# Optimization experiments

Hardware: AMD Instinct MI355X
Metric: run time of the kernel (lower is better)

Reference implementation:

```python
import jax, jax.numpy as jnp
import numpy as np

TEMP = 0.05
NUM_CLUSTERS = 8192  # labels.max()+1 in the original; fixed for jit-compat
EPS_SUM = 1e-6

def _l2norm(x):
    # F.normalize(x, dim=1): x / ||x||.clamp_min(1e-12)
    return x / jnp.maximum(jnp.linalg.norm(x, axis=1, keepdims=True), 1e-12)

def setup_inputs() -> dict:
    key = jax.random.key(0)
    k1, k2, k3, k4 = jax.random.split(key, 4)
    B, N, D = 1024, 131072, 256
    inputs = jax.random.normal(k1, (B, D), dtype=jnp.float32)
    features = jax.random.normal(k2, (N, D), dtype=jnp.float32)  # memory bank buffer
    indexes = jax.random.randint(k3, (B,), 0, N)
    labels = jax.random.randint(k4, (N,), 0, NUM_CLUSTERS)
    return {"inputs": inputs, "features": features, "indexes": indexes, "labels": labels}

def reference(inputs, features, indexes, labels):
    B = inputs.shape[0]
    inputs_norm = _l2norm(inputs)            # [B, D]
    features_norm = _l2norm(features)        # [N, D]
    # HM.forward: cosine similarity against the memory bank, then temperature
    logits = (inputs_norm @ features_norm.T) / TEMP          # [B, N]
    # label-grouped scatter-reduce: sim[c, b] = sum over samples s with label c of logits[b, s]
    sim = jax.ops.segment_sum(logits.T, labels, num_segments=NUM_CLUSTERS)  # [NC, B]
    nums = jax.ops.segment_sum(jnp.ones((labels.shape[0],), jnp.float32), labels,
                               num_segments=NUM_CLUSTERS)                   # [NC]
    mask = (nums > 0).astype(jnp.float32)                                   # [NC]
    denom = mask * nums + (1.0 - mask)
    sim = sim / denom[:, None]               # per-cluster mean similarity
    # masked softmax over clusters, per sample
    simT = sim.T                             # [B, NC]
    exps = jnp.exp(simT) * mask[None, :]
    p = exps / (jnp.sum(exps, axis=1, keepdims=True) + EPS_SUM)
    logp = jnp.log(p + 1e-6)                 # [B, NC]
    targets = labels[indexes]                # [B]
    loss = -jnp.mean(jnp.take_along_axis(logp, targets[:, None], axis=1))
    return loss
```

## Files before the change

kernel.cpp:

```cpp
#include <hip/hip_runtime.h>

#define BSZ   1024
#define NSZ   131072
#define DSZ   256
#define NC    8192
#define TEMPR 0.05f
#define CAP   64

typedef float f32x4_t __attribute__((ext_vector_type(4)));
typedef int   i32x4_t __attribute__((ext_vector_type(4)));

__device__ __forceinline__ unsigned short f2bf(float f) {
  unsigned u = __float_as_uint(f);
  u += 0x7fffu + ((u >> 16) & 1u);
  return (unsigned short)(u >> 16);
}

__device__ __forceinline__ void gload16(const unsigned short* g, unsigned short* l) {
  __builtin_amdgcn_global_load_lds(
      (const __attribute__((address_space(1))) unsigned int*)(g),
      (__attribute__((address_space(3))) unsigned int*)(l), 16, 0, 0);
}

#define ZERO_F4_COUNT 2308

__global__ __launch_bounds__(256) void k_norm(const float* __restrict__ in,
                                              unsigned short* __restrict__ anorm,
                                              float4* __restrict__ zero_region) {
  int gid  = blockIdx.x * 256 + threadIdx.x;
  if (gid < ZERO_F4_COUNT) zero_region[gid] = make_float4(0.f, 0.f, 0.f, 0.f);
  int wid  = gid >> 6;
  int lane = threadIdx.x & 63;
  float4 v = reinterpret_cast<const float4*>(in)[wid * 64 + lane];
  float ss = v.x * v.x + v.y * v.y + v.z * v.z + v.w * v.w;
#pragma unroll
  for (int off = 32; off; off >>= 1) ss += __shfl_xor(ss, off);
  float rn = 1.f / fmaxf(sqrtf(ss), 1e-12f);
  ushort4 ob = make_ushort4(f2bf(v.x * rn), f2bf(v.y * rn), f2bf(v.z * rn), f2bf(v.w * rn));
  reinterpret_cast<ushort4*>(anorm)[wid * 64 + lane] = ob;
}

__global__ __launch_bounds__(256) void k_fill(const int* __restrict__ labels,
                                              int* __restrict__ cnt,
                                              int* __restrict__ bucket) {
  int i = blockIdx.x * 256 + threadIdx.x;
  int lab = labels[i];
  int p = atomicAdd(&cnt[lab], 1);
  if (p < CAP) bucket[(lab << 6) + p] = i;
}

__global__ __launch_bounds__(256) void k_gather_sum(const float* __restrict__ feat,
                                                    const int* __restrict__ bucket,
                                                    const int* __restrict__ cnt,
                                                    unsigned short* __restrict__ cmean) {
  __shared__ float4 part[192];
  int c    = blockIdx.x;
  int lane = threadIdx.x & 63;
  int wv   = threadIdx.x >> 6;
  int n = cnt[c];
  n = n < CAP ? n : CAP;
  int j = wv + 4 * lane;
  int myidx = (j < n) ? bucket[(c << 6) + j] : 0;
  float4 acc = make_float4(0.f, 0.f, 0.f, 0.f);
  int iters = (n - wv + 3) >> 2;
  float4 v;
  if (iters > 0) {
    int s0 = __shfl(myidx, 0);
    v = reinterpret_cast<const float4*>(feat)[(size_t)s0 * 64 + lane];
  }
  for (int t = 0; t < iters; ++t) {
    float4 cur = v;
    if (t + 1 < iters) {
      int sn = __shfl(myidx, t + 1);
      v = reinterpret_cast<const float4*>(feat)[(size_t)sn * 64 + lane];
    }
    float ss = cur.x * cur.x + cur.y * cur.y + cur.z * cur.z + cur.w * cur.w;
#pragma unroll
    for (int off = 32; off; off >>= 1) ss += __shfl_xor(ss, off);
    float rn = 1.f / fmaxf(sqrtf(ss), 1e-12f);
    acc.x += cur.x * rn; acc.y += cur.y * rn; acc.z += cur.z * rn; acc.w += cur.w * rn;
  }
  if (wv > 0) part[(wv - 1) * 64 + lane] = acc;
  __syncthreads();
  if (wv == 0) {
    float4 p1 = part[lane], p2 = part[64 + lane], p3 = part[128 + lane];
    acc.x += p1.x + p2.x + p3.x;
    acc.y += p1.y + p2.y + p3.y;
    acc.z += p1.z + p2.z + p3.z;
    acc.w += p1.w + p2.w + p3.w;
    float den = n > 0 ? (float)n : 1.f;
    float sc = 1.f / (TEMPR * den);
    ushort4 ob = make_ushort4(f2bf(acc.x * sc), f2bf(acc.y * sc),
                              f2bf(acc.z * sc), f2bf(acc.w * sc));
    reinterpret_cast<ushort4*>(cmean)[c * 64 + lane] = ob;
  }
}

__global__ __launch_bounds__(256) void k_gemm(const unsigned short* __restrict__ A,
                                              const unsigned short* __restrict__ Bt,
                                              const int* __restrict__ cnt,
                                              const int* __restrict__ indexes,
                                              const int* __restrict__ labels,
                                              float* __restrict__ sumexp,
                                              float* __restrict__ tlogit,
                                              int* __restrict__ ticket,
                                              float* __restrict__ out) {
  __shared__ __align__(16) unsigned short a_lds[128 * 64];
  __shared__ __align__(16) unsigned short b_lds[128 * 64];
  __shared__ int t_lds[128];
  __shared__ float red[4];
  __shared__ int lastflag;

  const int tid  = threadIdx.x;
  const int bn0  = blockIdx.x * 128;
  const int bm0  = blockIdx.y * 128;
  const int lane = tid & 63;
  const int w    = tid >> 6;
  const int wr   = w >> 1, wc = w & 1;
  const int col16 = lane & 15, khalf = lane >> 4;

  if (tid < 128) t_lds[tid] = labels[indexes[bm0 + tid]];

  f32x4_t acc[4][4] = {};

#pragma unroll 1
  for (int kt = 0; kt < 4; ++kt) {
    const int k0 = kt * 64;
    __syncthreads();
#pragma unroll
    for (int j = 0; j < 4; ++j) {
      int c   = (j * 4 + w) * 64 + lane;
      int row = c >> 3;
      int lk  = (c & 7) ^ (row & 7);
      const unsigned short* gA = A  + (size_t)(bm0 + row) * DSZ + k0 + lk * 8;
      const unsigned short* gB = Bt + (size_t)(bn0 + row) * DSZ + k0 + lk * 8;
      gload16(gA, a_lds + (j * 4 + w) * 512);
      gload16(gB, b_lds + (j * 4 + w) * 512);
    }
    __syncthreads();

#pragma unroll
    for (int ks = 0; ks < 2; ++ks) {
      const int klocB = ks * 64 + khalf * 16;
      i32x4_t af[4], bf[4];
#pragma unroll
      for (int m = 0; m < 4; ++m) {
        int lr = wr * 64 + m * 16 + col16;
        int ab = (lr << 7) + (klocB ^ ((lr & 7) << 4));
        af[m] = *reinterpret_cast<const i32x4_t*>(reinterpret_cast<const char*>(a_lds) + ab);
      }
#pragma unroll
      for (int n = 0; n < 4; ++n) {
        int lc = wc * 64 + n * 16 + col16;
        int bb = (lc << 7) + (klocB ^ ((lc & 7) << 4));
        bf[n] = *reinterpret_cast<const i32x4_t*>(reinterpret_cast<const char*>(b_lds) + bb);
      }
#pragma unroll
      for (int m = 0; m < 4; ++m)
#pragma unroll
        for (int n = 0; n < 4; ++n)
          asm("v_mfma_f32_16x16x32_bf16 %0, %1, %2, %0" : "+v"(acc[m][n]) : "v"(af[m]), "v"(bf[n]));
    }
  }

#pragma unroll
  for (int m = 0; m < 4; ++m) {
    const int lr0 = wr * 64 + m * 16 + khalf * 4;
    float s0 = 0.f, s1 = 0.f, s2 = 0.f, s3 = 0.f;
#pragma unroll
    for (int n = 0; n < 4; ++n) {
      int gc = bn0 + wc * 64 + n * 16 + col16;
      float msk = cnt[gc] > 0 ? 1.f : 0.f;
      if (t_lds[lr0 + 0] == gc) tlogit[bm0 + lr0 + 0] = acc[m][n][0];
      if (t_lds[lr0 + 1] == gc) tlogit[bm0 + lr0 + 1] = acc[m][n][1];
      if (t_lds[lr0 + 2] == gc) tlogit[bm0 + lr0 + 2] = acc[m][n][2];
      if (t_lds[lr0 + 3] == gc) tlogit[bm0 + lr0 + 3] = acc[m][n][3];
      s0 += msk * __expf(acc[m][n][0]);
      s1 += msk * __expf(acc[m][n][1]);
      s2 += msk * __expf(acc[m][n][2]);
      s3 += msk * __expf(acc[m][n][3]);
    }
#pragma unroll
    for (int off = 1; off < 16; off <<= 1) {
      s0 += __shfl_xor(s0, off);
      s1 += __shfl_xor(s1, off);
      s2 += __shfl_xor(s2, off);
      s3 += __shfl_xor(s3, off);
    }
    if (col16 == 0) {
      atomicAdd(&sumexp[bm0 + lr0 + 0], s0);
      atomicAdd(&sumexp[bm0 + lr0 + 1], s1);
      atomicAdd(&sumexp[bm0 + lr0 + 2], s2);
      atomicAdd(&sumexp[bm0 + lr0 + 3], s3);
    }
  }

  __syncthreads();
  if (tid == 0) {
    int t = __hip_atomic_fetch_add(ticket, 1, __ATOMIC_ACQ_REL, __HIP_MEMORY_SCOPE_AGENT);
    lastflag = (t == 511);
  }
  __syncthreads();
  if (lastflag) {
    float lp = 0.f;
    for (int r = tid; r < BSZ; r += 256) {
      float tl = __uint_as_float(__hip_atomic_load((const unsigned*)&tlogit[r],
                                 __ATOMIC_RELAXED, __HIP_MEMORY_SCOPE_AGENT));
      float se = __uint_as_float(__hip_atomic_load((const unsigned*)&sumexp[r],
                                 __ATOMIC_RELAXED, __HIP_MEMORY_SCOPE_AGENT));
      float p = __expf(tl) / (se + 1e-6f);
      lp += logf(p + 1e-6f);
    }
#pragma unroll
    for (int off = 32; off; off >>= 1) lp += __shfl_xor(lp, off);
    if (lane == 0) red[w] = lp;
    __syncthreads();
    if (tid == 0) out[0] = -(red[0] + red[1] + red[2] + red[3]) * (1.0f / (float)BSZ);
  }
}

#define OFF_ANORM   0u
#define OFF_CMEAN   524288u
#define OFF_BUCKET  (OFF_CMEAN + 4194304u)
#define OFF_TLOGIT  (OFF_BUCKET + 2097152u)
#define OFF_CNT     (OFF_TLOGIT + 4096u)
#define OFF_SUMEXP  (OFF_CNT + 32768u)
#define OFF_TICKET  (OFF_SUMEXP + 4096u)

extern "C" void kernel_launch(void* const* d_in, const int* in_sizes, int n_in,
                              void* d_out, int out_size, void* d_ws, size_t ws_size,
                              hipStream_t stream) {
  const float* inputs   = (const float*)d_in[0];
  const float* features = (const float*)d_in[1];
  const int*   indexes  = (const int*)d_in[2];
  const int*   labels   = (const int*)d_in[3];
  float* out = (float*)d_out;

  char* ws = (char*)d_ws;
  unsigned short* anorm   = (unsigned short*)(ws + OFF_ANORM);
  unsigned short* cmean   = (unsigned short*)(ws + OFF_CMEAN);
  int*            bucket  = (int*)(ws + OFF_BUCKET);
  float*          tlogit  = (float*)(ws + OFF_TLOGIT);
  int*            cnt     = (int*)(ws + OFF_CNT);
  float*          sumexp  = (float*)(ws + OFF_SUMEXP);
  int*            ticket  = (int*)(ws + OFF_TICKET);

  k_norm<<<256, 256, 0, stream>>>(inputs, anorm, (float4*)(ws + OFF_CNT));
  k_fill<<<NSZ / 256, 256, 0, stream>>>(labels, cnt, bucket);
  k_gather_sum<<<NC, 256, 0, stream>>>(features, bucket, cnt, cmean);
  k_gemm<<<dim3(NC / 128, BSZ / 128), 256, 0, stream>>>(anorm, cmean, cnt, indexes,
                                                        labels, sumexp, tlogit,
                                                        ticket, out);
}
```

Baseline: 68.26 us.

## Double-buffer GEMM LDS tiles, vectorize label fill, two clusters per gather block

The GEMM kernel now double-buffers its A/B LDS tiles, issuing the global-to-LDS loads for the next K step before computing on the current one, so each iteration needs one barrier instead of two. k_fill loads labels as int4 and does four atomics per thread, launching a quarter of the blocks. k_gather_sum handles two clusters per block with interleaved loads to raise memory-level parallelism. The GEMM LDS footprint doubles, which may lower occupancy. Bucket insertion order changes, so the float summation order of the cluster means can differ.

```diff
diff --git a/kernel.cpp b/kernel.cpp
--- a/kernel.cpp
+++ b/kernel.cpp
@@ -43,56 +43,79 @@
 __global__ __launch_bounds__(256) void k_fill(const int* __restrict__ labels,
                                               int* __restrict__ cnt,
                                               int* __restrict__ bucket) {
-  int i = blockIdx.x * 256 + threadIdx.x;
-  int lab = labels[i];
-  int p = atomicAdd(&cnt[lab], 1);
-  if (p < CAP) bucket[(lab << 6) + p] = i;
+  int gid = blockIdx.x * 256 + threadIdx.x;
+  int4 l = reinterpret_cast<const int4*>(labels)[gid];
+  int base = gid * 4;
+  int p0 = atomicAdd(&cnt[l.x], 1);
+  int p1 = atomicAdd(&cnt[l.y], 1);
+  int p2 = atomicAdd(&cnt[l.z], 1);
+  int p3 = atomicAdd(&cnt[l.w], 1);
+  if (p0 < CAP) bucket[(l.x << 6) + p0] = base + 0;
+  if (p1 < CAP) bucket[(l.y << 6) + p1] = base + 1;
+  if (p2 < CAP) bucket[(l.z << 6) + p2] = base + 2;
+  if (p3 < CAP) bucket[(l.w << 6) + p3] = base + 3;
 }
 
 __global__ __launch_bounds__(256) void k_gather_sum(const float* __restrict__ feat,
                                                     const int* __restrict__ bucket,
                                                     const int* __restrict__ cnt,
                                                     unsigned short* __restrict__ cmean) {
-  __shared__ float4 part[192];
-  int c    = blockIdx.x;
-  int lane = threadIdx.x & 63;
-  int wv   = threadIdx.x >> 6;
-  int n = cnt[c];
-  n = n < CAP ? n : CAP;
+  __shared__ float4 part[2][192];
+  const int lane = threadIdx.x & 63;
+  const int wv   = threadIdx.x >> 6;
+  const int c0   = blockIdx.x * 2;
+  int n0 = cnt[c0];     n0 = n0 < CAP ? n0 : CAP;
+  int n1 = cnt[c0 + 1]; n1 = n1 < CAP ? n1 : CAP;
   int j = wv + 4 * lane;
-  int myidx = (j < n) ? bucket[(c << 6) + j] : 0;
-  float4 acc = make_float4(0.f, 0.f, 0.f, 0.f);
-  int iters = (n - wv + 3) >> 2;
-  float4 v;
-  if (iters > 0) {
-    int s0 = __shfl(myidx, 0);
-    v = reinterpret_cast<const float4*>(feat)[(size_t)s0 * 64 + lane];
-  }
-  for (int t = 0; t < iters; ++t) {
-    float4 cur = v;
-    if (t + 1 < iters) {
-      int sn = __shfl(myidx, t + 1);
-      v = reinterpret_cast<const float4*>(feat)[(size_t)sn * 64 + lane];
-    }
-    float ss = cur.x * cur.x + cur.y * cur.y + cur.z * cur.z + cur.w * cur.w;
-#pragma unroll
-    for (int off = 32; off; off >>= 1) ss += __shfl_xor(ss, off);
-    float rn = 1.f / fmaxf(sqrtf(ss), 1e-12f);
-    acc.x += cur.x * rn; acc.y += cur.y * rn; acc.z += cur.z * rn; acc.w += cur.w * rn;
-  }
-  if (wv > 0) part[(wv - 1) * 64 + lane] = acc;
+  int idx0 = (j < n0) ? bucket[(c0 << 6) + j] : 0;
+  int idx1 = (j < n1) ? bucket[((c0 + 1) << 6) + j] : 0;
+  float4 acc0 = make_float4(0.f, 0.f, 0.f, 0.f);
+  float4 acc1 = make_float4(0.f, 0.f, 0.f, 0.f);
+  int it0 = (n0 - wv + 3) >> 2;
+  int it1 = (n1 - wv + 3) >> 2;
+  int itm = it0 > it1 ? it0 : it1;
+  float4 v0, v1;
+  if (it0 > 0) { int s = __shfl(idx0, 0); v0 = reinterpret_cast<const float4*>(feat)[(size_t)s * 64 + lane]; }
+  if (it1 > 0) { int s = __shfl(idx1, 0); v1 = reinterpret_cast<const float4*>(feat)[(size_t)s * 64 + lane]; }
+  for (int t = 0; t < itm; ++t) {
+    float4 a = v0, b = v1;
+    if (t + 1 < it0) { int s = __shfl(idx0, t + 1); v0 = reinterpret_cast<const float4*>(feat)[(size_t)s * 64 + lane]; }
+    if (t + 1 < it1) { int s = __shfl(idx1, t + 1); v1 = reinterpret_cast<const float4*>(feat)[(size_t)s * 64 + lane]; }
+    if (t < it0) {
+      float ss = a.x * a.x + a.y * a.y + a.z * a.z + a.w * a.w;
+#pragma unroll
+      for (int off = 32; off; off >>= 1) ss += __shfl_xor(ss, off);
+      float rn = 1.f / fmaxf(sqrtf(ss), 1e-12f);
+      acc0.x += a.x * rn; acc0.y += a.y * rn; acc0.z += a.z * rn; acc0.w += a.w * rn;
+    }
+    if (t < it1) {
+      float ss = b.x * b.x + b.y * b.y + b.z * b.z + b.w * b.w;
+#pragma unroll
+      for (int off = 32; off; off >>= 1) ss += __shfl_xor(ss, off);
+      float rn = 1.f / fmaxf(sqrtf(ss), 1e-12f);
+      acc1.x += b.x * rn; acc1.y += b.y * rn; acc1.z += b.z * rn; acc1.w += b.w * rn;
+    }
+  }
+  if (wv > 0) {
+    part[0][(wv - 1) * 64 + lane] = acc0;
+    part[1][(wv - 1) * 64 + lane] = acc1;
+  }
   __syncthreads();
   if (wv == 0) {
-    float4 p1 = part[lane], p2 = part[64 + lane], p3 = part[128 + lane];
-    acc.x += p1.x + p2.x + p3.x;
-    acc.y += p1.y + p2.y + p3.y;
-    acc.z += p1.z + p2.z + p3.z;
-    acc.w += p1.w + p2.w + p3.w;
-    float den = n > 0 ? (float)n : 1.f;
-    float sc = 1.f / (TEMPR * den);
-    ushort4 ob = make_ushort4(f2bf(acc.x * sc), f2bf(acc.y * sc),
-                              f2bf(acc.z * sc), f2bf(acc.w * sc));
-    reinterpret_cast<ushort4*>(cmean)[c * 64 + lane] = ob;
+    float4 p1, p2, p3;
+    p1 = part[0][lane]; p2 = part[0][64 + lane]; p3 = part[0][128 + lane];
+    acc0.x += p1.x + p2.x + p3.x; acc0.y += p1.y + p2.y + p3.y;
+    acc0.z += p1.z + p2.z + p3.z; acc0.w += p1.w + p2.w + p3.w;
+    p1 = part[1][lane]; p2 = part[1][64 + lane]; p3 = part[1][128 + lane];
+    acc1.x += p1.x + p2.x + p3.x; acc1.y += p1.y + p2.y + p3.y;
+    acc1.z += p1.z + p2.z + p3.z; acc1.w += p1.w + p2.w + p3.w;
+    float d0 = n0 > 0 ? (float)n0 : 1.f;
+    float d1 = n1 > 0 ? (float)n1 : 1.f;
+    float s0 = 1.f / (TEMPR * d0), s1 = 1.f / (TEMPR * d1);
+    reinterpret_cast<ushort4*>(cmean)[c0 * 64 + lane] =
+        make_ushort4(f2bf(acc0.x * s0), f2bf(acc0.y * s0), f2bf(acc0.z * s0), f2bf(acc0.w * s0));
+    reinterpret_cast<ushort4*>(cmean)[(c0 + 1) * 64 + lane] =
+        make_ushort4(f2bf(acc1.x * s1), f2bf(acc1.y * s1), f2bf(acc1.z * s1), f2bf(acc1.w * s1));
   }
 }
 
@@ -105,8 +128,8 @@
                                               float* __restrict__ tlogit,
                                               int* __restrict__ ticket,
                                               float* __restrict__ out) {
-  __shared__ __align__(16) unsigned short a_lds[128 * 64];
-  __shared__ __align__(16) unsigned short b_lds[128 * 64];
+  __shared__ __align__(16) unsigned short a_lds[2][128 * 64];
+  __shared__ __align__(16) unsigned short b_lds[2][128 * 64];
   __shared__ int t_lds[128];
   __shared__ float red[4];
   __shared__ int lastflag;
@@ -121,24 +144,31 @@
 
   if (tid < 128) t_lds[tid] = labels[indexes[bm0 + tid]];
 
+  const int c_   = w * 64 + lane;
+#define STAGE(kt, buf)                                                        \
+  {                                                                           \
+    const int k0_ = (kt) * 64;                                                \
+    _Pragma("unroll")                                                         \
+    for (int jj = 0; jj < 4; ++jj) {                                          \
+      int c = jj * 256 + c_;                                                  \
+      int row = c >> 3;                                                       \
+      int lk = (c & 7) ^ (row & 7);                                           \
+      gload16(A + (size_t)(bm0 + row) * DSZ + k0_ + lk * 8,                   \
+              a_lds[buf] + (jj * 4 + w) * 512);                               \
+      gload16(Bt + (size_t)(bn0 + row) * DSZ + k0_ + lk * 8,                  \
+              b_lds[buf] + (jj * 4 + w) * 512);                               \
+    }                                                                         \
+  }
+
   f32x4_t acc[4][4] = {};
 
-#pragma unroll 1
+  STAGE(0, 0);
+  __syncthreads();
+
+#pragma unroll
   for (int kt = 0; kt < 4; ++kt) {
-    const int k0 = kt * 64;
-    __syncthreads();
-#pragma unroll
-    for (int j = 0; j < 4; ++j) {
-      int c   = (j * 4 + w) * 64 + lane;
-      int row = c >> 3;
-      int lk  = (c & 7) ^ (row & 7);
-      const unsigned short* gA = A  + (size_t)(bm0 + row) * DSZ + k0 + lk * 8;
-      const unsigned short* gB = Bt + (size_t)(bn0 + row) * DSZ + k0 + lk * 8;
-      gload16(gA, a_lds + (j * 4 + w) * 512);
-      gload16(gB, b_lds + (j * 4 + w) * 512);
-    }
-    __syncthreads();
-
+    const int cur = kt & 1;
+    if (kt < 3) STAGE(kt + 1, cur ^ 1);
 #pragma unroll
     for (int ks = 0; ks < 2; ++ks) {
       const int klocB = ks * 64 + khalf * 16;
@@ -147,13 +177,13 @@
       for (int m = 0; m < 4; ++m) {
         int lr = wr * 64 + m * 16 + col16;
         int ab = (lr << 7) + (klocB ^ ((lr & 7) << 4));
-        af[m] = *reinterpret_cast<const i32x4_t*>(reinterpret_cast<const char*>(a_lds) + ab);
+        af[m] = *reinterpret_cast<const i32x4_t*>(reinterpret_cast<const char*>(a_lds[cur]) + ab);
       }
 #pragma unroll
       for (int n = 0; n < 4; ++n) {
         int lc = wc * 64 + n * 16 + col16;
         int bb = (lc << 7) + (klocB ^ ((lc & 7) << 4));
-        bf[n] = *reinterpret_cast<const i32x4_t*>(reinterpret_cast<const char*>(b_lds) + bb);
+        bf[n] = *reinterpret_cast<const i32x4_t*>(reinterpret_cast<const char*>(b_lds[cur]) + bb);
       }
 #pragma unroll
       for (int m = 0; m < 4; ++m)
@@ -161,6 +191,7 @@
         for (int n = 0; n < 4; ++n)
           asm("v_mfma_f32_16x16x32_bf16 %0, %1, %2, %0" : "+v"(acc[m][n]) : "v"(af[m]), "v"(bf[n]));
     }
+    __syncthreads();
   }
 
 #pragma unroll
@@ -246,8 +277,8 @@
   int*            ticket  = (int*)(ws + OFF_TICKET);
 
   k_norm<<<256, 256, 0, stream>>>(inputs, anorm, (float4*)(ws + OFF_CNT));
-  k_fill<<<NSZ / 256, 256, 0, stream>>>(labels, cnt, bucket);
-  k_gather_sum<<<NC, 256, 0, stream>>>(features, bucket, cnt, cmean);
+  k_fill<<<NSZ / 1024, 256, 0, stream>>>(labels, cnt, bucket);
+  k_gather_sum<<<NC / 2, 256, 0, stream>>>(features, bucket, cnt, cmean);
   k_gemm<<<dim3(NC / 128, BSZ / 128), 256, 0, stream>>>(anorm, cmean, cnt, indexes,
                                                         labels, sumexp, tlogit,
                                                         ticket, out);
```

New measurement: 72.27 us. +5.9%, slower.
